# Kernel tuning notes

Measured on AMD Instinct MI355X. Metric: run time of the kernel, lower is better.

The kernel has to match this reference:

```python
import jax, jax.numpy as jnp
import numpy as np

B, T, E, H = 2, 2048, 1024, 16


def setup_inputs() -> dict:
    key = jax.random.key(0)
    ks = jax.random.split(key, 6)
    s = lambda k, shape: jax.random.normal(k, shape, dtype=jnp.float32) * 0.02
    return {
        "x": jax.random.normal(ks[0], (B, T, E), dtype=jnp.float32),
        "ln1_g": jnp.ones((E,), jnp.float32),
        "ln1_b": jnp.zeros((E,), jnp.float32),
        "attn_w": s(ks[1], (E, 3 * E)),
        "attn_b": jnp.zeros((3 * E,), jnp.float32),
        "proj_w": s(ks[2], (E, E)),
        "proj_b": jnp.zeros((E,), jnp.float32),
        "ln2_g": jnp.ones((E,), jnp.float32),
        "ln2_b": jnp.zeros((E,), jnp.float32),
        "mlp_w1": s(ks[3], (E, 4 * E)),
        "mlp_b1": jnp.zeros((4 * E,), jnp.float32),
        "mlp_w2": s(ks[4], (4 * E, E)),
        "mlp_b2": jnp.zeros((E,), jnp.float32),
        "w_att": jnp.ones((1,), jnp.float32),
        "w_mlp": jnp.ones((1,), jnp.float32),
    }


def _ln(x, g, b, eps=1e-5):
    m = x.mean(-1, keepdims=True)
    v = ((x - m) ** 2).mean(-1, keepdims=True)
    return (x - m) * jax.lax.rsqrt(v + eps) * g + b


def reference(x, ln1_g, ln1_b, attn_w, attn_b, proj_w, proj_b,
              ln2_g, ln2_b, mlp_w1, mlp_b1, mlp_w2, mlp_b2, w_att, w_mlp):
    Bx, Tx, Ex = x.shape
    hd = Ex // H
    # --- self-attention on ln_1(x) ---
    qkv = _ln(x, ln1_g, ln1_b) @ attn_w + attn_b          # [B,T,3E]
    q, k, v = jnp.split(qkv, 3, axis=-1)
    q = q.reshape(Bx, Tx, H, hd)
    k = k.reshape(Bx, Tx, H, hd)
    v = v.reshape(Bx, Tx, H, hd)
    att = jnp.einsum('bthd,bshd->bhts', q, k) * (1.0 / np.sqrt(hd))  # [B,H,T,T]
    causal = jnp.tril(jnp.ones((Tx, Tx), dtype=bool))
    att = jnp.where(causal, att, -jnp.inf)
    att = jax.nn.softmax(att, axis=-1)
    y = jnp.einsum('bhts,bshd->bthd', att, v).reshape(Bx, Tx, Ex)
    y = y @ proj_w + proj_b
    x = x * w_att + y
    # --- MLP on ln_2(x) ---
    h = _ln(x, ln2_g, ln2_b) @ mlp_w1 + mlp_b1
    h = jax.nn.gelu(h, approximate=False)
    x = x * w_mlp + (h @ mlp_w2 + mlp_b2)
    return x
```

## Files before the change

### kernel.cpp

```cpp
#include <hip/hip_runtime.h>
#include <math.h>

typedef __bf16 bf16;
typedef bf16 bf16x8 __attribute__((ext_vector_type(8)));
typedef bf16 bf16x4 __attribute__((ext_vector_type(4)));
typedef float f32x4 __attribute__((ext_vector_type(4)));

#define MFMA(a, b, c) __builtin_amdgcn_mfma_f32_16x16x32_bf16((a), (b), (c), 0, 0, 0)

#define GLOAD_LDS16(gp, lp)                                                        \
  __builtin_amdgcn_global_load_lds((const __attribute__((address_space(1))) void*)(gp), \
                                   (__attribute__((address_space(3))) void*)(lp), 16, 0, 0)

static const size_t E_WT_ATTN = 0;
static const size_t E_WT_PROJ = 3145728;
static const size_t E_WT_MLP1 = 4194304;
static const size_t E_WT_MLP2 = 8388608;
static const size_t E_LN1     = 12582912;
static const size_t E_QKV     = 16777216;
static const size_t E_VT      = 37748736;
static const size_t E_Y       = 41943040;
static const size_t E_LN2     = 46137344;
static const size_t E_H       = 50331648;
static const size_t BYTE_X2    = 134217728;
static const size_t BYTE_OPART = 150994944;
static const size_t BYTE_ML    = 184549376;
static const size_t BYTE_GPART = 185597952;
static const size_t TOTAL_BYTES = 252706816;

__device__ __align__(4096) unsigned char g_buf[TOTAL_BYTES];

__global__ __launch_bounds__(256) void transpose_cast(const float* __restrict__ in,
                                                      bf16* __restrict__ out, int K, int N) {
  __shared__ float tile[32][33];
  int bx = blockIdx.x, by = blockIdx.y;
  int tx = threadIdx.x, ty = threadIdx.y;
#pragma unroll
  for (int i = ty; i < 32; i += 8)
    tile[i][tx] = in[(size_t)(by * 32 + i) * N + bx * 32 + tx];
  __syncthreads();
#pragma unroll
  for (int i = ty; i < 32; i += 8)
    out[(size_t)(bx * 32 + i) * K + by * 32 + tx] = (bf16)tile[tx][i];
}

__global__ __launch_bounds__(256) void ln_bf16(const float* __restrict__ x,
                                               const float* __restrict__ g,
                                               const float* __restrict__ b,
                                               bf16* __restrict__ out) {
  int row = blockIdx.x, tid = threadIdx.x;
  const float* xr = x + ((size_t)row << 10);
  float4 v = *(const float4*)(xr + tid * 4);
  float s = v.x + v.y + v.z + v.w;
  float ss = v.x * v.x + v.y * v.y + v.z * v.z + v.w * v.w;
#pragma unroll
  for (int off = 32; off >= 1; off >>= 1) {
    s += __shfl_down(s, off);
    ss += __shfl_down(ss, off);
  }
  __shared__ float sh[8];
  int wid = tid >> 6;
  if ((tid & 63) == 0) { sh[wid] = s; sh[wid + 4] = ss; }
  __syncthreads();
  float ts = sh[0] + sh[1] + sh[2] + sh[3];
  float tss = sh[4] + sh[5] + sh[6] + sh[7];
  float mean = ts * (1.0f / 1024.0f);
  float var = tss * (1.0f / 1024.0f) - mean * mean;
  float inv = rsqrtf(var + 1e-5f);
  float4 gg = *(const float4*)(g + tid * 4);
  float4 bb = *(const float4*)(b + tid * 4);
  bf16x4 o;
  o[0] = (bf16)((v.x - mean) * inv * gg.x + bb.x);
  o[1] = (bf16)((v.y - mean) * inv * gg.y + bb.y);
  o[2] = (bf16)((v.z - mean) * inv * gg.z + bb.z);
  o[3] = (bf16)((v.w - mean) * inv * gg.w + bb.w);
  *(bf16x4*)(out + ((size_t)row << 10) + tid * 4) = o;
}

template <int EPI>
__global__ __launch_bounds__(256) void gemm_bt(const bf16* __restrict__ A,
                                               const bf16* __restrict__ Bt,
                                               const float* __restrict__ bias,
                                               bf16* __restrict__ outb,
                                               float* __restrict__ outf,
                                               int M, int N, int K, int Kseg) {
  __shared__ __align__(16) bf16 As[128 * 32];
  __shared__ __align__(16) bf16 Bs[128 * 32];
  int bx = blockIdx.x, by = blockIdx.y;
  int tid = threadIdx.x;
  int lane = tid & 63, wid = tid >> 6;
  int wr = wid >> 1, wc = wid & 1;
  int g = lane >> 4, lr = lane & 15;
  f32x4 acc[4][4];
#pragma unroll
  for (int m = 0; m < 4; ++m)
#pragma unroll
    for (int n = 0; n < 4; ++n) acc[m][n] = (f32x4){0.f, 0.f, 0.f, 0.f};
  const bf16* Ab = A + (size_t)by * 128 * K;
  const bf16* Bb = Bt + (size_t)bx * 128 * K;
  int srow = tid >> 2;
  int sk8 = (tid & 3) * 8;
  const bf16* Ap0 = Ab + (size_t)srow * K + sk8;
  const bf16* Ap1 = Ab + (size_t)(srow + 64) * K + sk8;
  const bf16* Bp0 = Bb + (size_t)srow * K + sk8;
  const bf16* Bp1 = Bb + (size_t)(srow + 64) * K + sk8;
  bf16* lA0 = As + tid * 8;
  bf16* lA1 = As + 2048 + tid * 8;
  bf16* lB0 = Bs + tid * 8;
  bf16* lB1 = Bs + 2048 + tid * 8;
  int kbeg = blockIdx.z * Kseg;
  int kend = kbeg + Kseg;
  for (int k0 = kbeg; k0 < kend; k0 += 32) {
    GLOAD_LDS16(Ap0 + k0, lA0);
    GLOAD_LDS16(Ap1 + k0, lA1);
    GLOAD_LDS16(Bp0 + k0, lB0);
    GLOAD_LDS16(Bp1 + k0, lB1);
    __syncthreads();
    bf16x8 af[4], bfv[4];
#pragma unroll
    for (int m = 0; m < 4; ++m) af[m] = *(const bf16x8*)(As + (wr * 64 + m * 16 + lr) * 32 + g * 8);
#pragma unroll
    for (int n = 0; n < 4; ++n) bfv[n] = *(const bf16x8*)(Bs + (wc * 64 + n * 16 + lr) * 32 + g * 8);
#pragma unroll
    for (int m = 0; m < 4; ++m)
#pragma unroll
      for (int n = 0; n < 4; ++n) acc[m][n] = MFMA(af[m], bfv[n], acc[m][n]);
    __syncthreads();
  }
  if (EPI == 3) {
    float* po = outf + (size_t)blockIdx.z * M * N;
#pragma unroll
    for (int m = 0; m < 4; ++m) {
#pragma unroll
      for (int n = 0; n < 4; ++n) {
        int rg0 = by * 128 + wr * 64 + m * 16 + g * 4;
        int cg = bx * 128 + wc * 64 + n * 16 + lr;
#pragma unroll
        for (int j = 0; j < 4; ++j) po[(size_t)(rg0 + j) * N + cg] = acc[m][n][j];
      }
    }
  } else {
#pragma unroll
    for (int m = 0; m < 4; ++m) {
#pragma unroll
      for (int n = 0; n < 4; ++n) {
        int rg0 = by * 128 + wr * 64 + m * 16 + g * 4;
        int cg = bx * 128 + wc * 64 + n * 16 + lr;
        float bv = bias[cg];
#pragma unroll
        for (int j = 0; j < 4; ++j) {
          float v = acc[m][n][j] + bv;
          size_t idx = (size_t)(rg0 + j) * N + cg;
          if (EPI == 0)
            outb[idx] = (bf16)v;
          else
            outb[idx] = (bf16)(0.5f * v * (1.0f + erff(v * 0.70710678118f)));
        }
      }
    }
  }
}

template <int SK>
__global__ __launch_bounds__(256) void reduce_add(const float* __restrict__ part,
                                                  const float* __restrict__ bias,
                                                  const float* __restrict__ res,
                                                  const float* __restrict__ wsc,
                                                  float* __restrict__ out, int MN, int N) {
  size_t i = ((size_t)blockIdx.x * 256 + threadIdx.x) * 4;
  float4 a = *(const float4*)(part + i);
#pragma unroll
  for (int s = 1; s < SK; ++s) {
    float4 b = *(const float4*)(part + (size_t)s * MN + i);
    a.x += b.x; a.y += b.y; a.z += b.z; a.w += b.w;
  }
  int col = (int)(i & (size_t)(N - 1));
  float4 bv = *(const float4*)(bias + col);
  float4 rv = *(const float4*)(res + i);
  float w = wsc[0];
  float4 o;
  o.x = rv.x * w + a.x + bv.x;
  o.y = rv.y * w + a.y + bv.y;
  o.z = rv.z * w + a.z + bv.z;
  o.w = rv.w * w + a.w + bv.w;
  *(float4*)(out + i) = o;
}

__global__ __launch_bounds__(256) void reduce_ln(const float* __restrict__ part,
                                                 const float* __restrict__ bias,
                                                 const float* __restrict__ res,
                                                 const float* __restrict__ wsc,
                                                 const float* __restrict__ lng,
                                                 const float* __restrict__ lnb,
                                                 float* __restrict__ x2out,
                                                 bf16* __restrict__ lnout) {
  int row = blockIdx.x, tid = threadIdx.x;
  size_t i = ((size_t)row << 10) + tid * 4;
  float4 a = *(const float4*)(part + i);
  float4 b2 = *(const float4*)(part + 4194304 + i);
  float4 rv = *(const float4*)(res + i);
  float4 bv = *(const float4*)(bias + tid * 4);
  float w = wsc[0];
  float4 o;
  o.x = rv.x * w + a.x + b2.x + bv.x;
  o.y = rv.y * w + a.y + b2.y + bv.y;
  o.z = rv.z * w + a.z + b2.z + bv.z;
  o.w = rv.w * w + a.w + b2.w + bv.w;
  *(float4*)(x2out + i) = o;
  float s = o.x + o.y + o.z + o.w;
  float ss = o.x * o.x + o.y * o.y + o.z * o.z + o.w * o.w;
#pragma unroll
  for (int off = 32; off >= 1; off >>= 1) {
    s += __shfl_down(s, off);
    ss += __shfl_down(ss, off);
  }
  __shared__ float sh[8];
  int wid = tid >> 6;
  if ((tid & 63) == 0) { sh[wid] = s; sh[wid + 4] = ss; }
  __syncthreads();
  float ts = sh[0] + sh[1] + sh[2] + sh[3];
  float tss = sh[4] + sh[5] + sh[6] + sh[7];
  float mean = ts * (1.0f / 1024.0f);
  float var = tss * (1.0f / 1024.0f) - mean * mean;
  float inv = rsqrtf(var + 1e-5f);
  float4 gg = *(const float4*)(lng + tid * 4);
  float4 bb = *(const float4*)(lnb + tid * 4);
  bf16x4 ov;
  ov[0] = (bf16)((o.x - mean) * inv * gg.x + bb.x);
  ov[1] = (bf16)((o.y - mean) * inv * gg.y + bb.y);
  ov[2] = (bf16)((o.z - mean) * inv * gg.z + bb.z);
  ov[3] = (bf16)((o.w - mean) * inv * gg.w + bb.w);
  *(bf16x4*)(lnout + ((size_t)row << 10) + tid * 4) = ov;
}

__global__ __launch_bounds__(256) void split_v_t(const bf16* __restrict__ qkv,
                                                 bf16* __restrict__ vT) {
  int t0 = blockIdx.x * 32;
  int bh = blockIdx.y;
  int b = bh >> 4, h = bh & 15;
  __shared__ bf16 tile[32][72];
  int tid = threadIdx.x;
  int d = tid & 63, tl0 = tid >> 6;
#pragma unroll
  for (int p = 0; p < 8; ++p) {
    int tl = p * 4 + tl0;
    tile[tl][d] = qkv[((size_t)(b * 2048 + t0 + tl)) * 3072 + 2048 + h * 64 + d];
  }
  __syncthreads();
  int tl = tid & 31, dq = tid >> 5;
#pragma unroll
  for (int p = 0; p < 8; ++p) {
    int dd = p * 8 + dq;
    vT[((size_t)(bh * 64 + dd)) * 2048 + t0 + tl] = tile[tl][dd];
  }
}

__global__ __launch_bounds__(256) void attn_fwd(const bf16* __restrict__ qkv,
                                                const bf16* __restrict__ vT,
                                                float* __restrict__ o_part,
                                                float* __restrict__ ml_part) {
  __shared__ __align__(16) bf16 Ks[2][4096];
  __shared__ __align__(16) bf16 Vs[2][4096];
  __shared__ bf16 P[4][16][72];
  int id = blockIdx.x;
  int bh = id & 31;
  int seg = (id >> 5) & 1;
  int qi = ((id >> 6) + bh) & 31;
  int tid = threadIdx.x, wid = tid >> 6, lane = tid & 63;
  int g = lane >> 4, lr = lane & 15;
  int b = bh >> 4, h = bh & 15;
  int nk = qi + 1;
  int n0 = (nk + 1) >> 1;
  int kt0 = seg ? n0 : 0;
  int kt1 = seg ? nk : n0;
  int qrow = qi * 64 + wid * 16 + lr;
  const bf16* Qr = qkv + ((size_t)(b * 2048 + qrow)) * 3072 + h * 64;
  bf16x8 qf[2];
  qf[0] = *(const bf16x8*)(Qr + g * 8);
  qf[1] = *(const bf16x8*)(Qr + 32 + g * 8);
  int r0 = tid >> 3, cs0 = ((tid & 7) ^ (r0 & 7)) << 3;
  int c1i = tid + 256;
  int r1 = c1i >> 3, cs1 = ((c1i & 7) ^ (r1 & 7)) << 3;
  const bf16* sK0 = qkv + ((size_t)(b * 2048 + r0)) * 3072 + 1024 + h * 64 + cs0;
  const bf16* sK1 = qkv + ((size_t)(b * 2048 + r1)) * 3072 + 1024 + h * 64 + cs1;
  const bf16* sV0 = vT + (size_t)bh * 131072 + (size_t)r0 * 2048 + cs0;
  const bf16* sV1 = vT + (size_t)bh * 131072 + (size_t)r1 * 2048 + cs1;
  bf16* dK0 = &Ks[0][0] + tid * 8;
  bf16* dK1 = &Ks[0][0] + 2048 + tid * 8;
  bf16* dV0 = &Vs[0][0] + tid * 8;
  bf16* dV1 = &Vs[0][0] + 2048 + tid * 8;
#define ATTN_STAGE(bufsel, ktv)                          \
  {                                                      \
    size_t kadv = (size_t)(ktv) * (64 * 3072);           \
    size_t vadv = (size_t)(ktv) * 64;                    \
    int bo = (bufsel) * 4096;                            \
    GLOAD_LDS16(sK0 + kadv, dK0 + bo);                   \
    GLOAD_LDS16(sK1 + kadv, dK1 + bo);                   \
    GLOAD_LDS16(sV0 + vadv, dV0 + bo);                   \
    GLOAD_LDS16(sV1 + vadv, dV1 + bo);                   \
  }
  f32x4 o[4];
#pragma unroll
  for (int n = 0; n < 4; ++n) o[n] = (f32x4){0.f, 0.f, 0.f, 0.f};
  float m = -3e38f, l = 0.f;
  if (kt0 < kt1) ATTN_STAGE(0, kt0);
  __syncthreads();
  const float beta = 0.18033688f;
  int sw = lr & 7;
  int sb = (lane & 48) | (g << 2);
  for (int kt = kt0; kt < kt1; ++kt) {
    int cur = (kt - kt0) & 1;
    if (kt + 1 < kt1) ATTN_STAGE(cur ^ 1, kt + 1);
    const bf16* Kb = &Ks[cur][0];
    const bf16* Vb = &Vs[cur][0];
    f32x4 s[4];
#pragma unroll
    for (int n = 0; n < 4; ++n) s[n] = (f32x4){0.f, 0.f, 0.f, 0.f};
#pragma unroll
    for (int kk = 0; kk < 2; ++kk) {
#pragma unroll
      for (int n = 0; n < 4; ++n) {
        bf16x8 kf = *(const bf16x8*)(Kb + ((n * 16 + lr) << 6) + ((((kk << 2) + g) ^ sw) << 3));
        s[n] = MFMA(kf, qf[kk], s[n]);
      }
    }
    int kc0 = kt * 64 + g * 4;
#pragma unroll
    for (int n = 0; n < 4; ++n)
#pragma unroll
      for (int j = 0; j < 4; ++j) {
        float sv = s[n][j] * beta;
        s[n][j] = ((kc0 + n * 16 + j) <= qrow) ? sv : -3e38f;
      }
    float mx = s[0][0];
#pragma unroll
    for (int n = 0; n < 4; ++n)
#pragma unroll
      for (int j = 0; j < 4; ++j) mx = fmaxf(mx, s[n][j]);
    mx = fmaxf(mx, __shfl_xor(mx, 16));
    mx = fmaxf(mx, __shfl_xor(mx, 32));
    float mn = fmaxf(m, mx);
    float al = exp2f(m - mn);
    m = mn;
    float rs = 0.f;
    bf16x4 pw[4];
#pragma unroll
    for (int n = 0; n < 4; ++n)
#pragma unroll
      for (int j = 0; j < 4; ++j) {
        float p = exp2f(s[n][j] - mn);
        rs += p;
        pw[n][j] = (bf16)p;
      }
    rs += __shfl_xor(rs, 16);
    rs += __shfl_xor(rs, 32);
    l = l * al + rs;
    float alj[4];
#pragma unroll
    for (int j = 0; j < 4; ++j) alj[j] = __shfl(al, sb + j);
#pragma unroll
    for (int n = 0; n < 4; ++n)
#pragma unroll
      for (int j = 0; j < 4; ++j) o[n][j] *= alj[j];
#pragma unroll
    for (int n = 0; n < 4; ++n) *(bf16x4*)&P[wid][lr][n * 16 + g * 4] = pw[n];
#pragma unroll
    for (int kk = 0; kk < 2; ++kk) {
      bf16x8 pf = *(const bf16x8*)&P[wid][lr][kk * 32 + g * 8];
#pragma unroll
      for (int n = 0; n < 4; ++n) {
        bf16x8 vf = *(const bf16x8*)(Vb + ((n * 16 + lr) << 6) + ((((kk << 2) + g) ^ sw) << 3));
        o[n] = MFMA(pf, vf, o[n]);
      }
    }
    __syncthreads();
  }
  float* ob = o_part + (size_t)id * 4096;
#pragma unroll
  for (int n = 0; n < 4; ++n)
#pragma unroll
    for (int j = 0; j < 4; ++j)
      ob[(size_t)(wid * 16 + g * 4 + j) * 64 + n * 16 + lr] = o[n][j];
  if (lane < 16) {
    ml_part[(size_t)id * 128 + (wid * 16 + lane) * 2] = m;
    ml_part[(size_t)id * 128 + (wid * 16 + lane) * 2 + 1] = l;
  }
#undef ATTN_STAGE
}

__global__ __launch_bounds__(256) void attn_combine(const float* __restrict__ o_part,
                                                    const float* __restrict__ ml_part,
                                                    bf16* __restrict__ y) {
  int c = blockIdx.x;
  int bh = c & 31, qi = c >> 5;
  int b = bh >> 4, h = bh & 15;
  int qraw = (qi - bh) & 31;
  size_t id0 = (size_t)bh + ((size_t)qraw << 6);
  size_t id1 = id0 + 32;
  int t = threadIdx.x;
  int r = t >> 2, cq = (t & 3) << 4;
  float m1 = ml_part[id0 * 128 + r * 2], l1 = ml_part[id0 * 128 + r * 2 + 1];
  float m2 = ml_part[id1 * 128 + r * 2], l2 = ml_part[id1 * 128 + r * 2 + 1];
  float mm = fmaxf(m1, m2);
  float w1 = exp2f(m1 - mm), w2 = exp2f(m2 - mm);
  float inv = 1.0f / (l1 * w1 + l2 * w2);
  const float* p1 = o_part + id0 * 4096 + r * 64 + cq;
  const float* p2 = o_part + id1 * 4096 + r * 64 + cq;
  bf16* yp = y + ((size_t)(b * 2048 + qi * 64 + r)) * 1024 + h * 64 + cq;
#pragma unroll
  for (int u = 0; u < 4; ++u) {
    float4 a = *(const float4*)(p1 + u * 4);
    float4 bq = *(const float4*)(p2 + u * 4);
    bf16x4 ov;
    ov[0] = (bf16)((a.x * w1 + bq.x * w2) * inv);
    ov[1] = (bf16)((a.y * w1 + bq.y * w2) * inv);
    ov[2] = (bf16)((a.z * w1 + bq.z * w2) * inv);
    ov[3] = (bf16)((a.w * w1 + bq.w * w2) * inv);
    *(bf16x4*)(yp + u * 4) = ov;
  }
}

extern "C" void kernel_launch(void* const* d_in, const int* in_sizes, int n_in,
                              void* d_out, int out_size, void* d_ws, size_t ws_size,
                              hipStream_t stream) {
  const float* x = (const float*)d_in[0];
  const float* ln1_g = (const float*)d_in[1];
  const float* ln1_b = (const float*)d_in[2];
  const float* attn_w = (const float*)d_in[3];
  const float* attn_b = (const float*)d_in[4];
  const float* proj_w = (const float*)d_in[5];
  const float* proj_b = (const float*)d_in[6];
  const float* ln2_g = (const float*)d_in[7];
  const float* ln2_b = (const float*)d_in[8];
  const float* mlp_w1 = (const float*)d_in[9];
  const float* mlp_b1 = (const float*)d_in[10];
  const float* mlp_w2 = (const float*)d_in[11];
  const float* mlp_b2 = (const float*)d_in[12];
  const float* w_att = (const float*)d_in[13];
  const float* w_mlp = (const float*)d_in[14];
  float* out = (float*)d_out;

  unsigned char* base = nullptr;
  if (ws_size >= TOTAL_BYTES) {
    base = (unsigned char*)d_ws;
  } else {
    hipGetSymbolAddress((void**)&base, HIP_SYMBOL(g_buf));
  }
  bf16* bb = (bf16*)base;
  bf16* wt_attn = bb + E_WT_ATTN;
  bf16* wt_proj = bb + E_WT_PROJ;
  bf16* wt_mlp1 = bb + E_WT_MLP1;
  bf16* wt_mlp2 = bb + E_WT_MLP2;
  bf16* ln1o = bb + E_LN1;
  bf16* qkv = bb + E_QKV;
  bf16* vTb = bb + E_VT;
  bf16* yb = bb + E_Y;
  bf16* ln2o = bb + E_LN2;
  bf16* hb = bb + E_H;
  float* x2 = (float*)(base + BYTE_X2);
  float* o_part = (float*)(base + BYTE_OPART);
  float* ml_part = (float*)(base + BYTE_ML);
  float* gpart = (float*)(base + BYTE_GPART);

  dim3 tb(32, 8);
  transpose_cast<<<dim3(3072 / 32, 1024 / 32), tb, 0, stream>>>(attn_w, wt_attn, 1024, 3072);
  transpose_cast<<<dim3(1024 / 32, 1024 / 32), tb, 0, stream>>>(proj_w, wt_proj, 1024, 1024);
  transpose_cast<<<dim3(4096 / 32, 1024 / 32), tb, 0, stream>>>(mlp_w1, wt_mlp1, 1024, 4096);
  transpose_cast<<<dim3(1024 / 32, 4096 / 32), tb, 0, stream>>>(mlp_w2, wt_mlp2, 4096, 1024);

  ln_bf16<<<4096, 256, 0, stream>>>(x, ln1_g, ln1_b, ln1o);

  gemm_bt<0><<<dim3(24, 32, 1), 256, 0, stream>>>(ln1o, wt_attn, attn_b, qkv, nullptr,
                                                  4096, 3072, 1024, 1024);

  split_v_t<<<dim3(64, 32), 256, 0, stream>>>(qkv, vTb);

  attn_fwd<<<2048, 256, 0, stream>>>(qkv, vTb, o_part, ml_part);
  attn_combine<<<1024, 256, 0, stream>>>(o_part, ml_part, yb);

  gemm_bt<3><<<dim3(8, 32, 2), 256, 0, stream>>>(yb, wt_proj, nullptr, nullptr, gpart,
                                                 4096, 1024, 1024, 512);
  reduce_ln<<<4096, 256, 0, stream>>>(gpart, proj_b, x, w_att, ln2_g, ln2_b, x2, ln2o);

  gemm_bt<1><<<dim3(32, 32, 1), 256, 0, stream>>>(ln2o, wt_mlp1, mlp_b1, hb, nullptr,
                                                  4096, 4096, 1024, 1024);

  gemm_bt<3><<<dim3(8, 32, 4), 256, 0, stream>>>(hb, wt_mlp2, nullptr, nullptr, gpart,
                                                 4096, 1024, 4096, 1024);
  reduce_add<4><<<4096, 256, 0, stream>>>(gpart, mlp_b2, x2, w_mlp, out, 4194304, 1024);
}
```

Baseline: 448.6 us.

## Add double-buffered 256x256 swizzled-LDS GEMM for QKV and MLP matmuls

Introduces a new GEMM kernel with 256x256 tiles, 512 threads, BK=64, and double-buffered LDS loads issued via global_load_lds. It applies an XOR swizzle to LDS columns to avoid bank conflicts and remaps block IDs for better L2 locality. The kernel replaces the 128x128 single-buffered GEMM for the QKV, MLP1 and MLP2 matmuls, while the projection GEMM keeps the old kernel in a specialised form. Larger tiles raise data reuse and overlap loads with MFMA, but they use 128KB of LDS and many accumulator registers, which limits occupancy, and the smaller grids may leave CUs underused.

Measured after the change: 404.0 us. 1.11x faster.

```diff
diff --git a/kernel.cpp b/kernel.cpp
--- a/kernel.cpp
+++ b/kernel.cpp
@@ -78,12 +78,107 @@
 }
 
 template <int EPI>
-__global__ __launch_bounds__(256) void gemm_bt(const bf16* __restrict__ A,
-                                               const bf16* __restrict__ Bt,
-                                               const float* __restrict__ bias,
-                                               bf16* __restrict__ outb,
-                                               float* __restrict__ outf,
-                                               int M, int N, int K, int Kseg) {
+__global__ __launch_bounds__(512, 2) void gemm256(const bf16* __restrict__ A,
+                                                  const bf16* __restrict__ Bt,
+                                                  const float* __restrict__ bias,
+                                                  bf16* __restrict__ outb,
+                                                  float* __restrict__ outf,
+                                                  int M, int N, int K, int Kseg) {
+  __shared__ __align__(16) bf16 As[2][16384];
+  __shared__ __align__(16) bf16 Bs[2][16384];
+  int tid = threadIdx.x;
+  int nwg = gridDim.x * gridDim.y;
+  int bid = blockIdx.y * gridDim.x + blockIdx.x;
+  int id2 = ((nwg & 7) == 0) ? ((bid & 7) * (nwg >> 3) + (bid >> 3)) : bid;
+  int bx = id2 % gridDim.x, by = id2 / gridDim.x;
+  int lane = tid & 63, wid = tid >> 6;
+  int wr = wid >> 2, wc = wid & 3;
+  int g = lane >> 4, lr = lane & 15;
+  f32x4 acc[8][4];
+#pragma unroll
+  for (int m = 0; m < 8; ++m)
+#pragma unroll
+    for (int n = 0; n < 4; ++n) acc[m][n] = (f32x4){0.f, 0.f, 0.f, 0.f};
+  const bf16* Ab = A + (size_t)by * 256 * K;
+  const bf16* Bb = Bt + (size_t)bx * 256 * K;
+  int rbase = tid >> 3;
+  int srccol = (((tid & 7) ^ (rbase & 7)) << 3);
+  const bf16* Asrc = Ab + (size_t)rbase * K + srccol;
+  const bf16* Bsrc = Bb + (size_t)rbase * K + srccol;
+#define G256_STAGE(buf, k0)                                                \
+  {                                                                        \
+    _Pragma("unroll") for (int q = 0; q < 4; ++q) {                        \
+      GLOAD_LDS16(Asrc + (size_t)(q * 64) * K + (k0), &As[buf][tid * 8 + q * 4096]); \
+      GLOAD_LDS16(Bsrc + (size_t)(q * 64) * K + (k0), &Bs[buf][tid * 8 + q * 4096]); \
+    }                                                                      \
+  }
+  int kbeg = blockIdx.z * Kseg;
+  int NT = Kseg >> 6;
+  G256_STAGE(0, kbeg);
+  __syncthreads();
+  int c = 0;
+  for (int t = 0; t < NT; ++t) {
+    if (t + 1 < NT) G256_STAGE(c ^ 1, kbeg + (t + 1) * 64);
+#pragma unroll
+    for (int kk = 0; kk < 2; ++kk) {
+      bf16x8 af[8], bfv[4];
+#pragma unroll
+      for (int m = 0; m < 8; ++m) {
+        int row = wr * 128 + m * 16 + lr;
+        af[m] = *(const bf16x8*)&As[c][row * 64 + ((((kk << 2) + g) ^ (row & 7)) << 3)];
+      }
+#pragma unroll
+      for (int n = 0; n < 4; ++n) {
+        int row = wc * 64 + n * 16 + lr;
+        bfv[n] = *(const bf16x8*)&Bs[c][row * 64 + ((((kk << 2) + g) ^ (row & 7)) << 3)];
+      }
+#pragma unroll
+      for (int m = 0; m < 8; ++m)
+#pragma unroll
+        for (int n = 0; n < 4; ++n) acc[m][n] = MFMA(af[m], bfv[n], acc[m][n]);
+    }
+    __syncthreads();
+    c ^= 1;
+  }
+#undef G256_STAGE
+  if (EPI == 3) {
+    float* po = outf + (size_t)blockIdx.z * M * N;
+#pragma unroll
+    for (int m = 0; m < 8; ++m) {
+#pragma unroll
+      for (int n = 0; n < 4; ++n) {
+        int rg0 = by * 256 + wr * 128 + m * 16 + g * 4;
+        int cg = bx * 256 + wc * 64 + n * 16 + lr;
+#pragma unroll
+        for (int j = 0; j < 4; ++j) po[(size_t)(rg0 + j) * N + cg] = acc[m][n][j];
+      }
+    }
+  } else {
+#pragma unroll
+    for (int m = 0; m < 8; ++m) {
+#pragma unroll
+      for (int n = 0; n < 4; ++n) {
+        int rg0 = by * 256 + wr * 128 + m * 16 + g * 4;
+        int cg = bx * 256 + wc * 64 + n * 16 + lr;
+        float bv = bias[cg];
+#pragma unroll
+        for (int j = 0; j < 4; ++j) {
+          float v = acc[m][n][j] + bv;
+          size_t idx = (size_t)(rg0 + j) * N + cg;
+          if (EPI == 0)
+            outb[idx] = (bf16)v;
+          else
+            outb[idx] = (bf16)(0.5f * v * (1.0f + erff(v * 0.70710678118f)));
+        }
+      }
+    }
+  }
+}
+
+__global__ __launch_bounds__(256) void gemm_bt3(const bf16* __restrict__ A,
+                                                const bf16* __restrict__ Bt,
+                                                float* __restrict__ outf,
+                                                int M, int N, int K, int Kseg) {
   __shared__ __align__(16) bf16 As[128 * 32];
   __shared__ __align__(16) bf16 Bs[128 * 32];
   int bx = blockIdx.x, by = blockIdx.y;
@@ -127,36 +222,15 @@
       for (int n = 0; n < 4; ++n) acc[m][n] = MFMA(af[m], bfv[n], acc[m][n]);
     __syncthreads();
   }
-  if (EPI == 3) {
-    float* po = outf + (size_t)blockIdx.z * M * N;
-#pragma unroll
-    for (int m = 0; m < 4; ++m) {
-#pragma unroll
-      for (int n = 0; n < 4; ++n) {
-        int rg0 = by * 128 + wr * 64 + m * 16 + g * 4;
-        int cg = bx * 128 + wc * 64 + n * 16 + lr;
-#pragma unroll
-        for (int j = 0; j < 4; ++j) po[(size_t)(rg0 + j) * N + cg] = acc[m][n][j];
-      }
-    }
-  } else {
-#pragma unroll
-    for (int m = 0; m < 4; ++m) {
-#pragma unroll
-      for (int n = 0; n < 4; ++n) {
-        int rg0 = by * 128 + wr * 64 + m * 16 + g * 4;
-        int cg = bx * 128 + wc * 64 + n * 16 + lr;
-        float bv = bias[cg];
-#pragma unroll
-        for (int j = 0; j < 4; ++j) {
-          float v = acc[m][n][j] + bv;
-          size_t idx = (size_t)(rg0 + j) * N + cg;
-          if (EPI == 0)
-            outb[idx] = (bf16)v;
-          else
-            outb[idx] = (bf16)(0.5f * v * (1.0f + erff(v * 0.70710678118f)));
-        }
-      }
+  float* po = outf + (size_t)blockIdx.z * M * N;
+#pragma unroll
+  for (int m = 0; m < 4; ++m) {
+#pragma unroll
+    for (int n = 0; n < 4; ++n) {
+      int rg0 = by * 128 + wr * 64 + m * 16 + g * 4;
+      int cg = bx * 128 + wc * 64 + n * 16 + lr;
+#pragma unroll
+      for (int j = 0; j < 4; ++j) po[(size_t)(rg0 + j) * N + cg] = acc[m][n][j];
     }
   }
 }
@@ -470,7 +544,7 @@
 
   ln_bf16<<<4096, 256, 0, stream>>>(x, ln1_g, ln1_b, ln1o);
 
-  gemm_bt<0><<<dim3(24, 32, 1), 256, 0, stream>>>(ln1o, wt_attn, attn_b, qkv, nullptr,
+  gemm256<0><<<dim3(12, 16, 1), 512, 0, stream>>>(ln1o, wt_attn, attn_b, qkv, nullptr,
                                                   4096, 3072, 1024, 1024);
 
   split_v_t<<<dim3(64, 32), 256, 0, stream>>>(qkv, vTb);
@@ -478,14 +552,13 @@
   attn_fwd<<<2048, 256, 0, stream>>>(qkv, vTb, o_part, ml_part);
   attn_combine<<<1024, 256, 0, stream>>>(o_part, ml_part, yb);
 
-  gemm_bt<3><<<dim3(8, 32, 2), 256, 0, stream>>>(yb, wt_proj, nullptr, nullptr, gpart,
-                                                 4096, 1024, 1024, 512);
+  gemm_bt3<<<dim3(8, 32, 2), 256, 0, stream>>>(yb, wt_proj, gpart, 4096, 1024, 1024, 512);
   reduce_ln<<<4096, 256, 0, stream>>>(gpart, proj_b, x, w_att, ln2_g, ln2_b, x2, ln2o);
 
-  gemm_bt<1><<<dim3(32, 32, 1), 256, 0, stream>>>(ln2o, wt_mlp1, mlp_b1, hb, nullptr,
+  gemm256<1><<<dim3(16, 16, 1), 512, 0, stream>>>(ln2o, wt_mlp1, mlp_b1, hb, nullptr,
                                                   4096, 4096, 1024, 1024);
 
-  gemm_bt<3><<<dim3(8, 32, 4), 256, 0, stream>>>(hb, wt_mlp2, nullptr, nullptr, gpart,
+  gemm256<3><<<dim3(4, 16, 4), 512, 0, stream>>>(hb, wt_mlp2, nullptr, nullptr, gpart,
                                                  4096, 1024, 4096, 1024);
   reduce_add<4><<<4096, 256, 0, stream>>>(gpart, mlp_b2, x2, w_mlp, out, 4194304, 1024);
 }
```
